# Optimization experiments

Measured on AMD Instinct MI355X. Metric: run time of the kernel, lower is better.

## Reference

```python
import jax, jax.numpy as jnp
import numpy as np

H = 16  # n_heads

def _rmsnorm(x, g, eps=1e-6):
    return x * jax.lax.rsqrt(jnp.mean(x * x, axis=-1, keepdims=True) + eps) * g

def _rope_diag(L, hd, dtype):
    # Diagonal of the full [L, hd, hd] rotary matrix: cos(pos * theta_pair) at every dim.
    # (The torch einsum 'bhld,ldd->bhld' extracts this diagonal, so no pairwise rotation occurs.)
    pair = jnp.arange(hd) // 2
    theta = 10000.0 ** (-2.0 * pair / hd)
    return jnp.cos(jnp.arange(L)[:, None].astype(jnp.float32) * theta[None, :]).astype(dtype)


def setup_inputs() -> dict:
    key = jax.random.key(0)
    ks = jax.random.split(key, 8)
    B, L, E = 2, 2048, 2048
    F = 2 * E  # SwiGLU width
    s = 0.02
    return {
        "x": jax.random.normal(ks[0], (B, L, E), jnp.float32),
        "g": jnp.ones((E,), jnp.float32),
        "wq": jax.random.normal(ks[1], (E, E), jnp.float32) * s,
        "wk": jax.random.normal(ks[2], (E, E), jnp.float32) * s,
        "wv": jax.random.normal(ks[3], (E, E), jnp.float32) * s,
        "w1": jax.random.normal(ks[4], (E, F), jnp.float32) * s,
        "b1": jnp.zeros((F,), jnp.float32),
        "wg": jax.random.normal(ks[5], (F, F), jnp.float32) * s,
        "bg": jnp.zeros((F,), jnp.float32),
        "wl": jax.random.normal(ks[6], (F, F), jnp.float32) * s,
        "bl": jnp.zeros((F,), jnp.float32),
        "beta": jnp.ones((1,), jnp.float32),
        "w2": jax.random.normal(ks[7], (F, E), jnp.float32) * s,
        "b2": jnp.zeros((E,), jnp.float32),
    }


def reference(x, g, wq, wk, wv, w1, b1, wg, bg, wl, bl, beta, w2, b2):
    B, L, E = x.shape
    hd = E // H
    x_res = x
    h = _rmsnorm(x, g)
    # projections -> [B, H, L, hd]
    q = (h @ wq).reshape(B, L, H, hd).transpose(0, 2, 1, 3)
    k = (h @ wk).reshape(B, L, H, hd).transpose(0, 2, 1, 3)
    v = (h @ wv).reshape(B, L, H, hd).transpose(0, 2, 1, 3)
    D = _rope_diag(L, hd, x.dtype)  # [L, hd], diagonal of rotary matrix
    q = q * D
    k = k * D
    score = jnp.einsum('bhld,bhmd->bhlm', q, k)  # [B,H,L,L]
    # causal mask added BEFORE scaling (faithful to source)
    mask = jnp.triu(jnp.full((L, L), -jnp.inf, dtype=score.dtype), k=1)
    score = (score + mask) / jnp.sqrt(jnp.asarray(hd, score.dtype))
    attn = jax.nn.softmax(score, axis=-1)
    o = jnp.einsum('bhlm,bhmd->bhld', attn, v)
    o = o.transpose(0, 2, 1, 3).reshape(B, L, E)
    x = o + x_res
    x_res = x
    h = _rmsnorm(x, g)
    h = h @ w1 + b1  # [B, L, 2E]
    gate = h @ wg + bg
    lin = h @ wl + bl
    act = gate * jax.nn.sigmoid(beta * gate) * lin
    out = act @ w2 + b2
    return out + x_res
```

## Files before the change

### kernel.cpp

```cpp
#include <hip/hip_runtime.h>
#include <cstdint>
#include <math.h>


typedef _Float16 f16;
typedef _Float16 f16x8 __attribute__((ext_vector_type(8)));
typedef _Float16 f16x4 __attribute__((ext_vector_type(4)));
typedef float    f32x4 __attribute__((ext_vector_type(4)));

#define MFMA_16x16x32(a, b, c) __builtin_amdgcn_mfma_f32_16x16x32_f16(a, b, c, 0, 0, 0)

__device__ __forceinline__ void gload_lds16(const void* g, void* lds) {
  __builtin_amdgcn_global_load_lds(
      (__attribute__((address_space(1))) void*)(uintptr_t)g,
      (__attribute__((address_space(3))) void*)(unsigned)(uintptr_t)lds,
      16, 0, 0);
}

__global__ void convT3_k(const float* __restrict__ W0, const float* __restrict__ W1,
                         const float* __restrict__ W2, f16* __restrict__ Wt) {
  __shared__ float tile[32][33];
  const int n0 = blockIdx.x << 5, k0 = blockIdx.y << 5, z = blockIdx.z;
  const float* W = (z == 0) ? W0 : (z == 1) ? W1 : W2;
  const int t = threadIdx.x;
  const int r = t >> 3, c4 = (t & 7) << 2;
  const f32x4 v = *(const f32x4*)(W + (size_t)(k0 + r) * 2048 + n0 + c4);
  tile[r][c4 + 0] = v[0]; tile[r][c4 + 1] = v[1];
  tile[r][c4 + 2] = v[2]; tile[r][c4 + 3] = v[3];
  __syncthreads();
  f16x4 o;
  o[0] = (f16)tile[c4 + 0][r]; o[1] = (f16)tile[c4 + 1][r];
  o[2] = (f16)tile[c4 + 2][r]; o[3] = (f16)tile[c4 + 3][r];
  *(f16x4*)(Wt + ((size_t)z * 2048 + n0 + r) * 2048 + k0 + c4) = o;
}

__global__ void convT_k(const float* __restrict__ W, f16* __restrict__ Wt,
                        int K, int N) {
  __shared__ float tile[32][33];
  const int n0 = blockIdx.x << 5, k0 = blockIdx.y << 5;
  const int t = threadIdx.x;
  const int r = t >> 3, c4 = (t & 7) << 2;
  const f32x4 v = *(const f32x4*)(W + (size_t)(k0 + r) * N + n0 + c4);
  tile[r][c4 + 0] = v[0]; tile[r][c4 + 1] = v[1];
  tile[r][c4 + 2] = v[2]; tile[r][c4 + 3] = v[3];
  __syncthreads();
  f16x4 o;
  o[0] = (f16)tile[c4 + 0][r]; o[1] = (f16)tile[c4 + 1][r];
  o[2] = (f16)tile[c4 + 2][r]; o[3] = (f16)tile[c4 + 3][r];
  *(f16x4*)(Wt + (size_t)(n0 + r) * K + k0 + c4) = o;
}

__global__ void convT_pack2_k(const float* __restrict__ Wg, const float* __restrict__ Wl,
                              f16* __restrict__ Wt) {
  __shared__ float tile[32][33];
  const int n0 = blockIdx.x << 5, k0 = blockIdx.y << 5, z = blockIdx.z;
  const float* W = z ? Wl : Wg;
  const int off = z << 7;
  const int t = threadIdx.x;
  const int r = t >> 3, c4 = (t & 7) << 2;
  const f32x4 v = *(const f32x4*)(W + (size_t)(k0 + r) * 4096 + n0 + c4);
  tile[r][c4 + 0] = v[0]; tile[r][c4 + 1] = v[1];
  tile[r][c4 + 2] = v[2]; tile[r][c4 + 3] = v[3];
  __syncthreads();
  f16x4 o;
  o[0] = (f16)tile[c4 + 0][r]; o[1] = (f16)tile[c4 + 1][r];
  o[2] = (f16)tile[c4 + 2][r]; o[3] = (f16)tile[c4 + 3][r];
  const int n = n0 + r;
  const int pr = ((n >> 7) << 8) + off + (n & 127);
  *(f16x4*)(Wt + (size_t)pr * 4096 + k0 + c4) = o;
}

__global__ void rope_tab_k(float* __restrict__ Dt) {
  const int l = blockIdx.x, d = threadIdx.x;
  const float th = __expf(-0.0719557841f * (float)(d & ~1));
  Dt[(l << 7) + d] = cosf((float)l * th);
}

__global__ void rmsnorm_k(const float* __restrict__ X, const float* __restrict__ G,
                          f16* __restrict__ H) {
  __shared__ float red[4];
  const int row = blockIdx.x, t = threadIdx.x;
  const float* xp = X + ((size_t)row << 11) + (t << 3);
  const f32x4 v0 = *(const f32x4*)xp;
  const f32x4 v1 = *(const f32x4*)(xp + 4);
  float ss = v0[0]*v0[0] + v0[1]*v0[1] + v0[2]*v0[2] + v0[3]*v0[3]
           + v1[0]*v1[0] + v1[1]*v1[1] + v1[2]*v1[2] + v1[3]*v1[3];
#pragma unroll
  for (int m = 1; m < 64; m <<= 1) ss += __shfl_xor(ss, m);
  if ((t & 63) == 0) red[t >> 6] = ss;
  __syncthreads();
  const float tot = red[0] + red[1] + red[2] + red[3];
  const float rs = rsqrtf(tot * (1.f / 2048.f) + 1e-6f);
  const float* gp = G + (t << 3);
  const f32x4 g0 = *(const f32x4*)gp, g1 = *(const f32x4*)(gp + 4);
  f16x8 o;
  o[0] = (f16)(v0[0]*rs*g0[0]); o[1] = (f16)(v0[1]*rs*g0[1]);
  o[2] = (f16)(v0[2]*rs*g0[2]); o[3] = (f16)(v0[3]*rs*g0[3]);
  o[4] = (f16)(v1[0]*rs*g1[0]); o[5] = (f16)(v1[1]*rs*g1[1]);
  o[6] = (f16)(v1[2]*rs*g1[2]); o[7] = (f16)(v1[3]*rs*g1[3]);
  *(f16x8*)(H + ((size_t)row << 11) + (t << 3)) = o;
}

__global__ void rmsnorm_h_k(const f16* __restrict__ X, const float* __restrict__ G,
                            f16* __restrict__ H) {
  __shared__ float red[4];
  const int row = blockIdx.x, t = threadIdx.x;
  const f16x8 v = *(const f16x8*)(X + ((size_t)row << 11) + (t << 3));
  float f[8];
#pragma unroll
  for (int i = 0; i < 8; ++i) f[i] = (float)v[i];
  float ss = 0.f;
#pragma unroll
  for (int i = 0; i < 8; ++i) ss += f[i] * f[i];
#pragma unroll
  for (int m = 1; m < 64; m <<= 1) ss += __shfl_xor(ss, m);
  if ((t & 63) == 0) red[t >> 6] = ss;
  __syncthreads();
  const float tot = red[0] + red[1] + red[2] + red[3];
  const float rs = rsqrtf(tot * (1.f / 2048.f) + 1e-6f);
  const float* gp = G + (t << 3);
  const f32x4 g0 = *(const f32x4*)gp, g1 = *(const f32x4*)(gp + 4);
  f16x8 o;
#pragma unroll
  for (int i = 0; i < 4; ++i) o[i] = (f16)(f[i] * rs * g0[i]);
#pragma unroll
  for (int i = 0; i < 4; ++i) o[4 + i] = (f16)(f[4 + i] * rs * g1[i]);
  *(f16x8*)(H + ((size_t)row << 11) + (t << 3)) = o;
}

__global__ void vtrans_k(const f16* __restrict__ V, f16* __restrict__ Vt) {
  __shared__ f16 tile[32][36];
  const int l0 = blockIdx.x << 5, d0 = blockIdx.y << 5, bh = blockIdx.z;
  const int b = bh >> 4, h = bh & 15;
  const int t = threadIdx.x;
  const int r = t >> 3, c4 = (t & 7) << 2;
  const f16x4 v = *(const f16x4*)(V + (size_t)((b << 11) + l0 + r) * 2048 + (h << 7) + d0 + c4);
  tile[r][c4 + 0] = v[0]; tile[r][c4 + 1] = v[1];
  tile[r][c4 + 2] = v[2]; tile[r][c4 + 3] = v[3];
  __syncthreads();
  f16x4 o;
  o[0] = tile[c4 + 0][r]; o[1] = tile[c4 + 1][r];
  o[2] = tile[c4 + 2][r]; o[3] = tile[c4 + 3][r];
  *(f16x4*)(Vt + (size_t)((bh << 7) + d0 + r) * 2048 + l0 + c4) = o;
}

template <int EPI>
__launch_bounds__(512, 2)
__global__ void gemm256_k(const f16* __restrict__ A, const f16* __restrict__ Bt,
                          void* __restrict__ Cout, int M, int N, int K,
                          const float* __restrict__ bias,
                          const float* __restrict__ bias2,
                          const float* __restrict__ betap) {
  __shared__ alignas(16) f16 lds[65536];
  const int t = threadIdx.x, lane = t & 63, w = t >> 6;
  const int wm = w >> 2, wn = w & 3;
  const int bm = blockIdx.y << 8, bn = blockIdx.x << 8;
  const int lh = lane & 15, lq = lane >> 4;
  const int NT = K >> 6;
  const int lrow = lane >> 3;
  const int lco  = ((lane & 7) ^ lrow) << 3;

  const f16* Agl = A  + (size_t)(bm + lrow) * K + lco;
  const f16* Bgl = Bt + (size_t)(bn + lrow) * K + lco;
  const int aw = w << 3;
  const int bw = w << 4;

  f32x4 acc[8][4] = {};
  f16x8 bf[4][2];

  auto stA = [&](int tile, int half) {
    const int d = (tile & 1) << 15;
    const int k0 = tile << 6;
    const int r0 = aw + (half << 6);
    gload_lds16(Agl + (size_t)r0 * K + k0, (void*)&lds[d + r0 * 64]);
    gload_lds16(Agl + (size_t)(r0 + 128) * K + k0, (void*)&lds[d + (r0 + 128) * 64]);
  };
  auto stB = [&](int tile, int half) {
    const int d = ((tile & 1) << 15) + 16384;
    const int k0 = tile << 6;
    const int r0 = bw + (half << 7);
    gload_lds16(Bgl + (size_t)r0 * K + k0, (void*)&lds[d + r0 * 64]);
    gload_lds16(Bgl + (size_t)(r0 + 8) * K + k0, (void*)&lds[d + (r0 + 8) * 64]);
  };
  auto ldA = [&](int d, int mi, int kk) {
    const int r = (wm << 7) + (mi << 4) + lh;
    return *(const f16x8*)&lds[(d << 15) + r * 64 + ((((kk << 2) + lq) ^ (lh & 7)) << 3)];
  };
  auto ldB = [&](int d, int ni, int kk) {
    const int r = (wn << 6) + (ni << 4) + lh;
    return *(const f16x8*)&lds[(d << 15) + 16384 + r * 64 + ((((kk << 2) + lq) ^ (lh & 7)) << 3)];
  };

  stB(0, 0); stB(0, 1); stA(0, 0); stA(0, 1);
  stB(1, 0); stB(1, 1); stA(1, 0);
  asm volatile("s_waitcnt vmcnt(6)" ::: "memory");
  __builtin_amdgcn_s_barrier();

  for (int tt = 0; tt < NT; tt += 2) {
    const bool pf = (tt + 2 < NT);
#pragma unroll
    for (int hf = 0; hf < 2; ++hf) {
#pragma unroll
      for (int ph = 0; ph < 4; ++ph) {
        f16x8 a0k0 = ldA(hf, 2 * ph, 0),     a0k1 = ldA(hf, 2 * ph, 1);
        f16x8 a1k0 = ldA(hf, 2 * ph + 1, 0), a1k1 = ldA(hf, 2 * ph + 1, 1);
        if (ph == 0) {
#pragma unroll
          for (int ni = 0; ni < 4; ++ni) {
            bf[ni][0] = ldB(hf, ni, 0); bf[ni][1] = ldB(hf, ni, 1);
          }
        }
        if (hf == 0) {
          if (ph == 0) stA(tt + 1, 1);
          else if (ph == 1) { if (pf) stB(tt + 2, 0); }
          else if (ph == 2) { if (pf) stB(tt + 2, 1); }
          else              { if (pf) stA(tt + 2, 0); }
        } else {
          if (ph == 0)      { if (pf) stA(tt + 2, 1); }
          else if (ph == 1) { if (pf) stB(tt + 3, 0); }
          else if (ph == 2) { if (pf) stB(tt + 3, 1); }
          else              { if (pf) stA(tt + 3, 0); }
        }
        __builtin_amdgcn_s_barrier();
        __builtin_amdgcn_s_setprio(1);
#pragma unroll
        for (int ni = 0; ni < 4; ++ni) {
          acc[2 * ph][ni]     = MFMA_16x16x32(a0k0, bf[ni][0], acc[2 * ph][ni]);
          acc[2 * ph][ni]     = MFMA_16x16x32(a0k1, bf[ni][1], acc[2 * ph][ni]);
          acc[2 * ph + 1][ni] = MFMA_16x16x32(a1k0, bf[ni][0], acc[2 * ph + 1][ni]);
          acc[2 * ph + 1][ni] = MFMA_16x16x32(a1k1, bf[ni][1], acc[2 * ph + 1][ni]);
        }
        __builtin_amdgcn_s_setprio(0);
        if (ph == 3) {
          if (hf == 0) {
            if (pf) asm volatile("s_waitcnt vmcnt(6)" ::: "memory");
            else    asm volatile("s_waitcnt vmcnt(0)" ::: "memory");
          } else if (pf) {
            asm volatile("s_waitcnt vmcnt(6)" ::: "memory");
          }
        }
        __builtin_amdgcn_s_barrier();
      }
    }
  }

  if (EPI == 2) {
#pragma unroll
    for (int mi = 0; mi < 8; ++mi) {
#pragma unroll
      for (int ni = 0; ni < 4; ++ni) {
#pragma unroll
        for (int r = 0; r < 4; ++r) {
          const int grow = bm + (wm << 7) + (mi << 4) + (lq << 2) + r;
          const int gcol = bn + (wn << 6) + (ni << 4) + lh;
          ((f16*)Cout)[(size_t)grow * N + gcol] = (f16)(acc[mi][ni][r] + bias[gcol]);
        }
      }
    }
  } else {
    f16* linlds = (f16*)lds;
    const int ncol0 = bn >> 1;
    const int Nout = N >> 1;
    if (wn >= 2) {
#pragma unroll
      for (int mi = 0; mi < 8; ++mi)
#pragma unroll
        for (int ni = 0; ni < 4; ++ni)
#pragma unroll
          for (int r = 0; r < 4; ++r) {
            const int row = (wm << 7) + (mi << 4) + (lq << 2) + r;
            const int col = ((wn - 2) << 6) + (ni << 4) + lh;
            linlds[row * 136 + col] = (f16)(acc[mi][ni][r] + bias2[ncol0 + col]);
          }
    }
    __syncthreads();
    if (wn < 2) {
      const float be = betap[0];
#pragma unroll
      for (int mi = 0; mi < 8; ++mi)
#pragma unroll
        for (int ni = 0; ni < 4; ++ni)
#pragma unroll
          for (int r = 0; r < 4; ++r) {
            const int row = (wm << 7) + (mi << 4) + (lq << 2) + r;
            const int col = (wn << 6) + (ni << 4) + lh;
            const float v = acc[mi][ni][r] + bias[ncol0 + col];
            const float lin = (float)linlds[row * 136 + col];
            const float a = v / (1.f + __expf(-be * v)) * lin;
            ((f16*)Cout)[(size_t)(bm + row) * Nout + ncol0 + col] = (f16)a;
          }
    }
  }
}

template <int EPI>
__launch_bounds__(256, 3)
__global__ void gemm_k(const f16* __restrict__ A, const f16* __restrict__ Bt,
                       void* __restrict__ Cout, int M, int N, int K,
                       const float* __restrict__ bias,
                       const float* __restrict__ auxf,
                       const f16* __restrict__ auxh,
                       float scale) {
  __shared__ alignas(16) f16 As[128 * 64];
  __shared__ alignas(16) f16 Bs[128 * 64];
  const int t = threadIdx.x;
  const int lane = t & 63;
  const int w = t >> 6;
  const int wm = w >> 1, wn = w & 1;
  const int bm = blockIdx.y << 7;
  const int bn = blockIdx.x << 7;
  const int lh = lane & 15, lq = lane >> 4;

  f32x4 acc[4][4] = {};

  for (int k0 = 0; k0 < K; k0 += 64) {
    __syncthreads();
#pragma unroll
    for (int i = 0; i < 4; ++i) {
      const int idx = i * 256 + (w << 6) + lane;
      const int row = idx >> 3, c = idx & 7;
      const int cs = (c ^ (row & 7)) << 3;
      gload_lds16(A + (size_t)(bm + row) * K + k0 + cs,
                  &As[(i * 256 + (w << 6)) << 3]);
      gload_lds16(Bt + (size_t)(bn + row) * K + k0 + cs,
                  &Bs[(i * 256 + (w << 6)) << 3]);
    }
    asm volatile("s_waitcnt vmcnt(0)" ::: "memory");
    __syncthreads();
#pragma unroll
    for (int kk = 0; kk < 2; ++kk) {
      f16x8 af[4], bfr[4];
#pragma unroll
      for (int mi = 0; mi < 4; ++mi) {
        const int r = (wm << 6) + (mi << 4) + lh;
        af[mi] = *(const f16x8*)&As[(r << 6) + ((((kk << 2) + lq) ^ (r & 7)) << 3)];
      }
#pragma unroll
      for (int ni = 0; ni < 4; ++ni) {
        const int r = (wn << 6) + (ni << 4) + lh;
        bfr[ni] = *(const f16x8*)&Bs[(r << 6) + ((((kk << 2) + lq) ^ (r & 7)) << 3)];
      }
#pragma unroll
      for (int mi = 0; mi < 4; ++mi)
#pragma unroll
        for (int ni = 0; ni < 4; ++ni)
          acc[mi][ni] = MFMA_16x16x32(af[mi], bfr[ni], acc[mi][ni]);
    }
  }

#pragma unroll
  for (int mi = 0; mi < 4; ++mi) {
#pragma unroll
    for (int ni = 0; ni < 4; ++ni) {
#pragma unroll
      for (int r = 0; r < 4; ++r) {
        const int grow = bm + (wm << 6) + (mi << 4) + (lq << 2) + r;
        const int gcol = bn + (wn << 6) + (ni << 4) + lh;
        float v = acc[mi][ni][r];
        if (EPI == 6) {
          const int seg = gcol >> 11, c = gcol & 2047;
          if (seg < 2) {
            const float f = auxf[((grow & 2047) << 7) + (c & 127)];
            v *= (seg == 0) ? scale * f : f;
          }
          ((f16*)Cout)[(size_t)seg * 8388608 + ((size_t)grow << 11) + c] = (f16)v;
        } else {
          ((float*)Cout)[(size_t)grow * N + gcol] = v + bias[gcol] + (float)auxh[(size_t)grow * N + gcol];
        }
      }
    }
  }
}

__launch_bounds__(256, 2)
__global__ void attn_k(const f16* __restrict__ Q, const f16* __restrict__ Kb,
                       const f16* __restrict__ Vt, const float* __restrict__ Xres,
                       f16* __restrict__ X2, int* __restrict__ qcnt) {
  constexpr int L = 2048, E = 2048, HD = 128;
  __shared__ alignas(16) f16 Ks[2][64 * 128];
  __shared__ alignas(16) f16 Vs[128 * 64];
  __shared__ alignas(16) f16 Ps[4][32 * 72];
  __shared__ int s_item;

  const int t = threadIdx.x, lane = t & 63, w = t >> 6;
  const int lh = lane & 15, lq = lane >> 4;

  for (;;) {
    if (t == 0) s_item = atomicAdd(qcnt, 1);
    __syncthreads();
    const int item = s_item;
    if (item >= 512) return;
    const int bh = item & 31;
    const int q0 = (15 - (item >> 5)) << 7;
    const int b = bh >> 4, h = bh & 15;
    const int wrow0 = q0 + (w << 5);

    auto issueK = [&](int kv0, int buf) {
#pragma unroll
      for (int i = 0; i < 4; ++i) {
        const int idx = i * 256 + (w << 6) + lane;
        const int row = idx >> 4, c = idx & 15;
        gload_lds16(Kb + (size_t)(b * L + kv0 + row) * E + h * HD + ((c ^ (row & 7)) << 3),
                    &Ks[buf][(i * 256 + (w << 6)) << 3]);
      }
    };
    auto issueV = [&](int kv0) {
#pragma unroll
      for (int i = 0; i < 4; ++i) {
        const int idx = i * 256 + (w << 6) + lane;
        const int row = idx >> 3, c = idx & 7;
        gload_lds16(Vt + ((size_t)bh * HD + row) * L + kv0 + ((c ^ (row & 7)) << 3),
                    &Vs[(i * 256 + (w << 6)) << 3]);
      }
    };

    f16x8 qf[2][4];
#pragma unroll
    for (int mi = 0; mi < 2; ++mi) {
      const f16* qrow = Q + (size_t)(b * L + wrow0 + (mi << 4) + lh) * E + h * HD;
#pragma unroll
      for (int kq = 0; kq < 4; ++kq)
        qf[mi][kq] = *(const f16x8*)(qrow + (kq << 5) + (lq << 3));
    }
    asm volatile("s_waitcnt vmcnt(0)" ::: "memory");

    f32x4 oacc[2][8] = {};
    float mrun[2][4], lrun[2][4];
#pragma unroll
    for (int mi = 0; mi < 2; ++mi)
#pragma unroll
      for (int r = 0; r < 4; ++r) { mrun[mi][r] = -1e30f; lrun[mi][r] = 0.f; }

    const int nt = (q0 + 128) >> 6;
    issueK(0, 0);
    for (int it = 0; it < nt; ++it) {
      const int cur = it & 1;
      const int kv0 = it << 6;
      const bool more = (it + 1 < nt);
      issueV(kv0);
      if (more) {
        issueK(kv0 + 64, cur ^ 1);
        asm volatile("s_waitcnt vmcnt(8)" ::: "memory");
      } else {
        asm volatile("s_waitcnt vmcnt(4)" ::: "memory");
      }
      __builtin_amdgcn_s_barrier();

      const bool active = (kv0 <= wrow0 + 31);
      if (active) {
        f32x4 sacc[2][4] = {};
        __builtin_amdgcn_s_setprio(1);
#pragma unroll
        for (int kq = 0; kq < 4; ++kq) {
          f16x8 kf[4];
#pragma unroll
          for (int ni = 0; ni < 4; ++ni) {
            const int r = (ni << 4) + lh;
            kf[ni] = *(const f16x8*)&Ks[cur][(r << 7) + ((((kq << 2) + lq) ^ (r & 7)) << 3)];
          }
#pragma unroll
          for (int mi = 0; mi < 2; ++mi)
#pragma unroll
            for (int ni = 0; ni < 4; ++ni)
              sacc[mi][ni] = MFMA_16x16x32(qf[mi][kq], kf[ni], sacc[mi][ni]);
        }
        __builtin_amdgcn_s_setprio(0);
        if (kv0 + 63 > wrow0) {
#pragma unroll
          for (int mi = 0; mi < 2; ++mi)
#pragma unroll
            for (int ni = 0; ni < 4; ++ni)
#pragma unroll
              for (int r = 0; r < 4; ++r) {
                const int qr = wrow0 + (mi << 4) + (lq << 2) + r;
                const int kv = kv0 + (ni << 4) + lh;
                if (kv > qr) sacc[mi][ni][r] = -1e30f;
              }
        }
        float scl[2][4], rsum[2][4];
#pragma unroll
        for (int mi = 0; mi < 2; ++mi)
#pragma unroll
          for (int r = 0; r < 4; ++r) {
            float v = fmaxf(fmaxf(sacc[mi][0][r], sacc[mi][1][r]),
                            fmaxf(sacc[mi][2][r], sacc[mi][3][r]));
            v = fmaxf(v, __shfl_xor(v, 1));
            v = fmaxf(v, __shfl_xor(v, 2));
            v = fmaxf(v, __shfl_xor(v, 4));
            v = fmaxf(v, __shfl_xor(v, 8));
            const float mnew = fmaxf(mrun[mi][r], v);
            scl[mi][r] = __expf(mrun[mi][r] - mnew);
            mrun[mi][r] = mnew;
            rsum[mi][r] = 0.f;
          }
#pragma unroll
        for (int mi = 0; mi < 2; ++mi)
#pragma unroll
          for (int ni = 0; ni < 4; ++ni)
#pragma unroll
            for (int r = 0; r < 4; ++r) {
              const float p = __expf(sacc[mi][ni][r] - mrun[mi][r]);
              rsum[mi][r] += p;
              Ps[w][((mi << 4) + (lq << 2) + r) * 72 + (ni << 4) + lh] = (f16)p;
            }
#pragma unroll
        for (int mi = 0; mi < 2; ++mi)
#pragma unroll
          for (int r = 0; r < 4; ++r) {
            float s = rsum[mi][r];
            s += __shfl_xor(s, 1);
            s += __shfl_xor(s, 2);
            s += __shfl_xor(s, 4);
            s += __shfl_xor(s, 8);
            lrun[mi][r] = lrun[mi][r] * scl[mi][r] + s;
          }
#pragma unroll
        for (int mi = 0; mi < 2; ++mi)
#pragma unroll
          for (int nd = 0; nd < 8; ++nd)
#pragma unroll
            for (int r = 0; r < 4; ++r) oacc[mi][nd][r] *= scl[mi][r];
      }

      if (more) asm volatile("s_waitcnt vmcnt(4)" ::: "memory");
      else      asm volatile("s_waitcnt vmcnt(0)" ::: "memory");
      __builtin_amdgcn_s_barrier();

      if (active) {
        __builtin_amdgcn_s_setprio(1);
#pragma unroll
        for (int kp = 0; kp < 2; ++kp) {
          f16x8 pf[2];
#pragma unroll
          for (int mi = 0; mi < 2; ++mi)
            pf[mi] = *(const f16x8*)&Ps[w][((mi << 4) + lh) * 72 + (kp << 5) + (lq << 3)];
#pragma unroll
          for (int nd = 0; nd < 8; ++nd) {
            const int r = (nd << 4) + lh;
            const f16x8 vf = *(const f16x8*)&Vs[(r << 6) + ((((kp << 2) + lq) ^ (r & 7)) << 3)];
#pragma unroll
            for (int mi = 0; mi < 2; ++mi)
              oacc[mi][nd] = MFMA_16x16x32(pf[mi], vf, oacc[mi][nd]);
          }
        }
        __builtin_amdgcn_s_setprio(0);
      }
      asm volatile("" ::: "memory");
      __builtin_amdgcn_s_barrier();
    }
#pragma unroll
    for (int mi = 0; mi < 2; ++mi)
#pragma unroll
      for (int nd = 0; nd < 8; ++nd)
#pragma unroll
        for (int r = 0; r < 4; ++r) {
          const int qr = wrow0 + (mi << 4) + (lq << 2) + r;
          const size_t off = (size_t)(b * L + qr) * E + h * HD + (nd << 4) + lh;
          X2[off] = (f16)(oacc[mi][nd][r] / lrun[mi][r] + Xres[off]);
        }
  }
}

extern "C" void kernel_launch(void* const* d_in, const int* in_sizes, int n_in,
                              void* d_out, int out_size, void* d_ws, size_t ws_size,
                              hipStream_t stream) {
  const float* x    = (const float*)d_in[0];
  const float* g    = (const float*)d_in[1];
  const float* wq   = (const float*)d_in[2];
  const float* wk   = (const float*)d_in[3];
  const float* wv   = (const float*)d_in[4];
  const float* w1   = (const float*)d_in[5];
  const float* b1   = (const float*)d_in[6];
  const float* wgp  = (const float*)d_in[7];
  const float* bg   = (const float*)d_in[8];
  const float* wl   = (const float*)d_in[9];
  const float* bl   = (const float*)d_in[10];
  const float* beta = (const float*)d_in[11];
  const float* w2   = (const float*)d_in[12];
  const float* b2   = (const float*)d_in[13];

  constexpr size_t MB = 1ull << 20;
  char* ws = (char*)d_ws;
  f16*   wBIG = (f16*)(ws + 0 * MB);
  float* Dt   = (float*)(ws + 64 * MB);
  int*   qcnt = (int*)(ws + 65 * MB);
  f16*   hbuf = (f16*)(ws + 66 * MB);
  f16*   qkv  = (f16*)(ws + 82 * MB);
  f16*   vbuf = (f16*)(ws + 114 * MB);
  f16*   vtb  = (f16*)(ws + 130 * MB);
  f16*   x2h  = (f16*)(ws + 146 * MB);
  f16*   a1   = (f16*)(ws + 82 * MB);
  f16*   act  = (f16*)(ws + 114 * MB);
  (void)ws_size; (void)n_in; (void)in_sizes; (void)out_size;

  const dim3 blk(256);
  const float qscale = 0.08838834764831845f;

  rope_tab_k<<<2048, 128, 0, stream>>>(Dt);
  rmsnorm_k<<<4096, blk, 0, stream>>>(x, g, hbuf);
  hipMemsetAsync(qcnt, 0, 4, stream);

  convT3_k<<<dim3(64, 64, 3), blk, 0, stream>>>(wq, wk, wv, wBIG);
  gemm_k<6><<<dim3(48, 32), blk, 0, stream>>>(hbuf, wBIG, qkv, 4096, 6144, 2048,
                                              nullptr, Dt, nullptr, qscale);
  vtrans_k<<<dim3(64, 4, 32), blk, 0, stream>>>(vbuf, vtb);

  attn_k<<<384, blk, 0, stream>>>(qkv, qkv + (size_t)8388608, vtb, x, x2h, qcnt);

  rmsnorm_h_k<<<4096, blk, 0, stream>>>(x2h, g, hbuf);

  convT_k<<<dim3(128, 64), blk, 0, stream>>>(w1, wBIG, 2048, 4096);
  gemm256_k<2><<<dim3(16, 16), 512, 0, stream>>>(hbuf, wBIG, a1, 4096, 4096, 2048,
                                                 b1, nullptr, nullptr);
  convT_pack2_k<<<dim3(128, 128, 2), blk, 0, stream>>>(wgp, wl, wBIG);
  gemm256_k<7><<<dim3(32, 16), 512, 0, stream>>>(a1, wBIG, act, 4096, 8192, 4096,
                                                 bg, bl, beta);
  convT_k<<<dim3(64, 128), blk, 0, stream>>>(w2, wBIG, 4096, 2048);
  gemm_k<5><<<dim3(16, 32), blk, 0, stream>>>(act, wBIG, (float*)d_out, 4096, 2048, 4096,
                                              b2, nullptr, x2h, 1.0f);
}
```

Before: 712.1 us.

## Split long causal attention query tiles into two KV halves with merge kernel

Query tiles 8-15 are now split into two work items that each process half of the KV range. Each half writes unnormalized partial outputs plus running max and sum to workspace, and a new merge kernel combines them with residual add. This is meant to balance the triangular causal workload across the persistent grid, which grows from 384 to 512 blocks. The cost is extra f16 partial-output traffic, an extra launch, and rounding the partial outputs to f16.

```diff
diff --git a/kernel.cpp b/kernel.cpp
--- a/kernel.cpp
+++ b/kernel.cpp
@@ -372,10 +372,30 @@
   }
 }
 
+__device__ __forceinline__ void decode_item(int i, int& q, int& half, bool& split) {
+  if      (i < 64)  { q = 15; split = true;  half = (i >> 5) & 1; }
+  else if (i < 96)  { q = 7;  split = false; half = 0; }
+  else if (i < 160) { q = 14; split = true;  half = ((i - 96) >> 5) & 1; }
+  else if (i < 224) { q = 13; split = true;  half = ((i - 160) >> 5) & 1; }
+  else if (i < 256) { q = 6;  split = false; half = 0; }
+  else if (i < 320) { q = 12; split = true;  half = ((i - 256) >> 5) & 1; }
+  else if (i < 384) { q = 11; split = true;  half = ((i - 320) >> 5) & 1; }
+  else if (i < 416) { q = 5;  split = false; half = 0; }
+  else if (i < 480) { q = 10; split = true;  half = ((i - 416) >> 5) & 1; }
+  else if (i < 544) { q = 9;  split = true;  half = ((i - 480) >> 5) & 1; }
+  else if (i < 576) { q = 4;  split = false; half = 0; }
+  else if (i < 640) { q = 8;  split = true;  half = ((i - 576) >> 5) & 1; }
+  else if (i < 672) { q = 3;  split = false; half = 0; }
+  else if (i < 704) { q = 2;  split = false; half = 0; }
+  else if (i < 736) { q = 1;  split = false; half = 0; }
+  else              { q = 0;  split = false; half = 0; }
+}
+
 __launch_bounds__(256, 2)
 __global__ void attn_k(const f16* __restrict__ Q, const f16* __restrict__ Kb,
                        const f16* __restrict__ Vt, const float* __restrict__ Xres,
-                       f16* __restrict__ X2, int* __restrict__ qcnt) {
+                       f16* __restrict__ X2, int* __restrict__ qcnt,
+                       f16* __restrict__ OM, float* __restrict__ ML) {
   constexpr int L = 2048, E = 2048, HD = 128;
   __shared__ alignas(16) f16 Ks[2][64 * 128];
   __shared__ alignas(16) f16 Vs[128 * 64];
@@ -389,11 +409,22 @@
     if (t == 0) s_item = atomicAdd(qcnt, 1);
     __syncthreads();
     const int item = s_item;
-    if (item >= 512) return;
+    if (item >= 768) return;
+    int q, half; bool split;
+    decode_item(item, q, half, split);
     const int bh = item & 31;
-    const int q0 = (15 - (item >> 5)) << 7;
+    const int q0 = q << 7;
     const int b = bh >> 4, h = bh & 15;
     const int wrow0 = q0 + (w << 5);
+    int kv_lo, kv_hi;
+    if (split) {
+      const int mid = (q + 1) << 6;
+      kv_lo = half ? mid : 0;
+      kv_hi = half ? (mid << 1) : mid;
+    } else {
+      kv_lo = 0;
+      kv_hi = q0 + 128;
+    }
 
     auto issueK = [&](int kv0, int buf) {
 #pragma unroll
@@ -431,11 +462,11 @@
 #pragma unroll
       for (int r = 0; r < 4; ++r) { mrun[mi][r] = -1e30f; lrun[mi][r] = 0.f; }
 
-    const int nt = (q0 + 128) >> 6;
-    issueK(0, 0);
+    const int nt = (kv_hi - kv_lo) >> 6;
+    issueK(kv_lo, 0);
     for (int it = 0; it < nt; ++it) {
       const int cur = it & 1;
-      const int kv0 = it << 6;
+      const int kv0 = kv_lo + (it << 6);
       const bool more = (it + 1 < nt);
       issueV(kv0);
       if (more) {
@@ -548,16 +579,72 @@
       asm volatile("" ::: "memory");
       __builtin_amdgcn_s_barrier();
     }
-#pragma unroll
-    for (int mi = 0; mi < 2; ++mi)
-#pragma unroll
-      for (int nd = 0; nd < 8; ++nd)
-#pragma unroll
-        for (int r = 0; r < 4; ++r) {
-          const int qr = wrow0 + (mi << 4) + (lq << 2) + r;
-          const size_t off = (size_t)(b * L + qr) * E + h * HD + (nd << 4) + lh;
-          X2[off] = (f16)(oacc[mi][nd][r] / lrun[mi][r] + Xres[off]);
-        }
+
+    if (!split) {
+#pragma unroll
+      for (int mi = 0; mi < 2; ++mi)
+#pragma unroll
+        for (int nd = 0; nd < 8; ++nd)
+#pragma unroll
+          for (int r = 0; r < 4; ++r) {
+            const int qr = wrow0 + (mi << 4) + (lq << 2) + r;
+            const size_t off = (size_t)(b * L + qr) * E + h * HD + (nd << 4) + lh;
+            X2[off] = (f16)(oacc[mi][nd][r] / lrun[mi][r] + Xres[off]);
+          }
+    } else {
+      const int pidx = ((((q - 8) << 5) + bh) << 1) + half;
+      f16* Op = OM + (size_t)pidx * 16384;
+#pragma unroll
+      for (int mi = 0; mi < 2; ++mi)
+#pragma unroll
+        for (int nd = 0; nd < 8; ++nd)
+#pragma unroll
+          for (int r = 0; r < 4; ++r) {
+            const int row = (w << 5) + (mi << 4) + (lq << 2) + r;
+            Op[row * 128 + (nd << 4) + lh] = (f16)oacc[mi][nd][r];
+          }
+      if (lh == 0) {
+#pragma unroll
+        for (int mi = 0; mi < 2; ++mi)
+#pragma unroll
+          for (int r = 0; r < 4; ++r) {
+            const int row = (w << 5) + (mi << 4) + (lq << 2) + r;
+            ML[(pidx << 8) + (row << 1)]     = mrun[mi][r];
+            ML[(pidx << 8) + (row << 1) + 1] = lrun[mi][r];
+          }
+      }
+    }
+  }
+}
+
+__global__ void attn_merge_k(const f16* __restrict__ OM, const float* __restrict__ ML,
+                             const float* __restrict__ Xres, f16* __restrict__ X2) {
+  const int p = blockIdx.x;
+  const int q = 8 + (p >> 5), bh = p & 31;
+  const int b = bh >> 4, h = bh & 15;
+  const int t = threadIdx.x;
+  const f16* O1 = OM + (size_t)(p * 2) * 16384;
+  const f16* O2 = O1 + 16384;
+  const float* ml1 = ML + (size_t)(p * 2) * 256;
+  const float* ml2 = ml1 + 256;
+#pragma unroll
+  for (int pass = 0; pass < 8; ++pass) {
+    const int e = (pass << 8) + t;
+    const int row = e >> 4;
+    const int c0 = (e & 15) << 3;
+    const float m1 = ml1[row << 1], l1 = ml1[(row << 1) + 1];
+    const float m2 = ml2[row << 1], l2 = ml2[(row << 1) + 1];
+    const float m = fmaxf(m1, m2);
+    const float a1 = __expf(m1 - m), a2 = __expf(m2 - m);
+    const float inv = 1.f / (a1 * l1 + a2 * l2);
+    const f16x8 o1 = *(const f16x8*)&O1[row * 128 + c0];
+    const f16x8 o2 = *(const f16x8*)&O2[row * 128 + c0];
+    const size_t off = (size_t)(b * 2048 + (q << 7) + row) * 2048 + (h << 7) + c0;
+    f16x8 out;
+#pragma unroll
+    for (int j = 0; j < 8; ++j)
+      out[j] = (f16)((a1 * (float)o1[j] + a2 * (float)o2[j]) * inv + Xres[off + j]);
+    *(f16x8*)&X2[off] = out;
   }
 }
 
@@ -584,9 +671,11 @@
   f16*   wBIG = (f16*)(ws + 0 * MB);
   float* Dt   = (float*)(ws + 64 * MB);
   int*   qcnt = (int*)(ws + 65 * MB);
+  float* ML   = (float*)(ws + 65 * MB + 4096);
   f16*   hbuf = (f16*)(ws + 66 * MB);
   f16*   qkv  = (f16*)(ws + 82 * MB);
   f16*   vbuf = (f16*)(ws + 114 * MB);
+  f16*   OM   = (f16*)(ws + 114 * MB);
   f16*   vtb  = (f16*)(ws + 130 * MB);
   f16*   x2h  = (f16*)(ws + 146 * MB);
   f16*   a1   = (f16*)(ws + 82 * MB);
@@ -605,7 +694,8 @@
                                               nullptr, Dt, nullptr, qscale);
   vtrans_k<<<dim3(64, 4, 32), blk, 0, stream>>>(vbuf, vtb);
 
-  attn_k<<<384, blk, 0, stream>>>(qkv, qkv + (size_t)8388608, vtb, x, x2h, qcnt);
+  attn_k<<<512, blk, 0, stream>>>(qkv, qkv + (size_t)8388608, vtb, x, x2h, qcnt, OM, ML);
+  attn_merge_k<<<256, blk, 0, stream>>>(OM, ML, x, x2h);
 
   rmsnorm_h_k<<<4096, blk, 0, stream>>>(x2h, g, hbuf);
 
```

Result: slower. 755.0 us (+6.0%).
